# Performance work log

Measured on AMD Instinct MI355X. Metric: run time of the kernel, lower is better.

The kernel has to match this reference:

```python
import jax, jax.numpy as jnp
import numpy as np

HEAD_DIM = 32
KERNEL = 3
DILATION = 2
PAD = DILATION * (KERNEL - 1) // 2  # = 2
SCALE = HEAD_DIM ** (-0.5)


def _unfold(x):
    """Emulate nn.Unfold(kernel_size=KERNEL, dilation=DILATION, padding=PAD, stride=1).
    x: [B, C, H, W] -> [B, C, K*K, H, W] (channel-major, kernel positions inner,
    matching torch's C*K*K channel layout after the module's reshape)."""
    B, C, H, W = x.shape
    xp = jnp.pad(x, ((0, 0), (0, 0), (PAD, PAD), (PAD, PAD)))
    patches = [xp[:, :, i * DILATION:i * DILATION + H, j * DILATION:j * DILATION + W]
               for i in range(KERNEL) for j in range(KERNEL)]
    return jnp.stack(patches, axis=2)  # [B, C, K2, H, W]


def setup_inputs() -> dict:
    key = jax.random.key(0)
    kq, kk, kv = jax.random.split(key, 3)
    B, d, H, W = 4, 384, 64, 64
    q = jax.random.normal(kq, (B, d, H, W), dtype=jnp.float32)
    k = jax.random.normal(kk, (B, d, H, W), dtype=jnp.float32)
    v = jax.random.normal(kv, (B, d, H, W), dtype=jnp.float32)
    return {"q": q, "k": k, "v": v}


def reference(q, k, v):
    B, d, H, W = q.shape
    nh = d // HEAD_DIM
    K2 = KERNEL * KERNEL
    L = H * W
    # q: [B, nh, hd, L]
    qh = q.reshape(B, nh, HEAD_DIM, L)
    # unfolded k, v: [B, nh, hd, K2, L]
    ku = _unfold(k).reshape(B, nh, HEAD_DIM, K2, L)
    vu = _unfold(v).reshape(B, nh, HEAD_DIM, K2, L)
    # per-pixel attention logits: [B, nh, L, K2]
    attn = jnp.einsum('bncl,bnckl->bnlk', qh, ku) * SCALE
    attn = jax.nn.softmax(attn, axis=-1)
    # weighted values: [B, nh, L, hd]
    out = jnp.einsum('bnlk,bnckl->bnlc', attn, vu)
    # -> [B, L, nh, hd] -> [B, H, W, d]
    return out.transpose(0, 2, 1, 3).reshape(B, H, W, d)
```

## Files before the change

kernel.cpp:

```cpp
#include <hip/hip_runtime.h>


#define NHD  12
#define DDIM 384
#define HH   64
#define WW   64
#define HWSZ 4096
#define SCALEF 0.17677669529663687f

__global__ __launch_bounds__(256) void dilate_attn(const float* __restrict__ q,
                                                   const float* __restrict__ k,
                                                   const float* __restrict__ v,
                                                   float* __restrict__ out) {
    const int tid = threadIdx.x;
    const int r   = tid >> 6;
    const int x   = tid & 63;
    const int bz  = blockIdx.x;
    const int bh  = bz >> 4;
    const int b   = bh / NHD;
    const int n   = bh - b * NHD;
    const int y   = (bz & 15) * 4 + r;

    const int cbase = (b * DDIM + n * 32) * HWSZ;
    const int pix   = y * WW + x;

    int  rowoff[3];
    bool vy[3];
#pragma unroll
    for (int di = 0; di < 3; ++di) {
        int yy = y + 2 * di - 2;
        vy[di] = (yy >= 0) && (yy < HH);
        yy = yy < 0 ? 0 : (yy > 63 ? 63 : yy);
        rowoff[di] = yy * WW + x;
    }
    const bool vxm = (x >= 2);
    const bool vxp = (x <= 61);
    bool tval[9];
#pragma unroll
    for (int di = 0; di < 3; ++di) {
        tval[di * 3 + 0] = vy[di] && vxm;
        tval[di * 3 + 1] = vy[di];
        tval[di * 3 + 2] = vy[di] && vxp;
    }

    float qreg[32];
#pragma unroll
    for (int c = 0; c < 32; ++c) qreg[c] = q[cbase + pix + c * HWSZ] * SCALEF;

    float l[9];
#pragma unroll
    for (int t = 0; t < 9; ++t) l[t] = 0.f;
#pragma unroll
    for (int c = 0; c < 32; ++c) {
        const int base = cbase + c * HWSZ;
        const float qc = qreg[c];
#pragma unroll
        for (int di = 0; di < 3; ++di) {
            const float kc = k[base + rowoff[di]];
            const float km = __shfl_up(kc, 2);
            const float kp = __shfl_down(kc, 2);
            l[di * 3 + 0] += qc * km;
            l[di * 3 + 1] += qc * kc;
            l[di * 3 + 2] += qc * kp;
        }
    }

#pragma unroll
    for (int t = 0; t < 9; ++t) l[t] = tval[t] ? l[t] : 0.f;
    float m = l[0];
#pragma unroll
    for (int t = 1; t < 9; ++t) m = fmaxf(m, l[t]);
    float w[9], s = 0.f;
#pragma unroll
    for (int t = 0; t < 9; ++t) { w[t] = __expf(l[t] - m); s += w[t]; }
    float inv = 1.0f / s;
#pragma unroll
    for (int t = 0; t < 9; ++t) w[t] = tval[t] ? (w[t] * inv) : 0.f;

    float o[32];
#pragma unroll
    for (int c = 0; c < 32; ++c) o[c] = 0.f;
#pragma unroll
    for (int c = 0; c < 32; ++c) {
        const int base = cbase + c * HWSZ;
        float acc = 0.f;
#pragma unroll
        for (int di = 0; di < 3; ++di) {
            const float vc = v[base + rowoff[di]];
            const float vm = __shfl_up(vc, 2);
            const float vp = __shfl_down(vc, 2);
            acc += w[di * 3 + 0] * vm + w[di * 3 + 1] * vc + w[di * 3 + 2] * vp;
        }
        o[c] = acc;
    }

    const int ob = (b * HH * WW + pix) * DDIM + n * 32;
#pragma unroll
    for (int j = 0; j < 8; ++j)
        *(float4*)(out + ob + j * 4) =
            make_float4(o[j * 4], o[j * 4 + 1], o[j * 4 + 2], o[j * 4 + 3]);
}

extern "C" void kernel_launch(void* const* d_in, const int* in_sizes, int n_in,
                              void* d_out, int out_size, void* d_ws, size_t ws_size,
                              hipStream_t stream) {
    const float* q = (const float*)d_in[0];
    const float* k = (const float*)d_in[1];
    const float* v = (const float*)d_in[2];
    float* out = (float*)d_out;
    hipLaunchKernelGGL(dilate_attn, dim3(768), dim3(256), 0, stream, q, k, v, out);
}
```

Before: 124.7 us.

## Split channels across lane groups with float4 pixel loads and XCD-aware block remap

Each wave now covers one row with 16 lanes of 4 consecutive pixels each, and the 32 head channels are split into four groups of 8 across lane quarters. Loads of q, k and v become float4. Partial logits are reduced with xor shuffles across the channel groups, and neighbour taps come from shuffles of float4 components. The block index is also remapped so that consecutive logical blocks spread across the 8 XCDs. The intent is to raise memory-access width and cut per-thread register pressure, at the cost of extra shuffle reductions, and the output stores now write only 8 channels per pixel.

```diff
diff --git a/kernel.cpp b/kernel.cpp
--- a/kernel.cpp
+++ b/kernel.cpp
@@ -12,17 +12,23 @@
                                                    const float* __restrict__ k,
                                                    const float* __restrict__ v,
                                                    float* __restrict__ out) {
-    const int tid = threadIdx.x;
-    const int r   = tid >> 6;
-    const int x   = tid & 63;
-    const int bz  = blockIdx.x;
-    const int bh  = bz >> 4;
-    const int b   = bh / NHD;
-    const int n   = bh - b * NHD;
-    const int y   = (bz & 15) * 4 + r;
+    const int tid  = threadIdx.x;
+    const int lane = tid & 63;
+    const int i16  = lane & 15;
+    const int cg   = (lane >> 4) & 3;
+    const int wv   = tid >> 6;
+    const int x0   = i16 * 4;
 
-    const int cbase = (b * DDIM + n * 32) * HWSZ;
-    const int pix   = y * WW + x;
+    const int phys = blockIdx.x;
+    const int lz   = (phys & 7) * 96 + (phys >> 3);
+
+    const int bh = lz >> 4;
+    const int y  = (lz & 15) * 4 + wv;
+    const int b  = bh / NHD;
+    const int n  = bh - b * NHD;
+
+    const int cbase = (b * DDIM + n * 32 + cg * 8) * HWSZ;
+    const int prow  = y * WW;
 
     int  rowoff[3];
     bool vy[3];
@@ -31,74 +37,100 @@
         int yy = y + 2 * di - 2;
         vy[di] = (yy >= 0) && (yy < HH);
         yy = yy < 0 ? 0 : (yy > 63 ? 63 : yy);
-        rowoff[di] = yy * WW + x;
-    }
-    const bool vxm = (x >= 2);
-    const bool vxp = (x <= 61);
-    bool tval[9];
-#pragma unroll
-    for (int di = 0; di < 3; ++di) {
-        tval[di * 3 + 0] = vy[di] && vxm;
-        tval[di * 3 + 1] = vy[di];
-        tval[di * 3 + 2] = vy[di] && vxp;
+        rowoff[di] = yy * WW + x0;
     }
 
-    float qreg[32];
+    float4 qv[8];
 #pragma unroll
-    for (int c = 0; c < 32; ++c) qreg[c] = q[cbase + pix + c * HWSZ] * SCALEF;
+    for (int c = 0; c < 8; ++c) {
+        float4 t = *(const float4*)(q + cbase + c * HWSZ + prow + x0);
+        qv[c] = make_float4(t.x * SCALEF, t.y * SCALEF, t.z * SCALEF, t.w * SCALEF);
+    }
 
-    float l[9];
+    float l[4][9];
 #pragma unroll
-    for (int t = 0; t < 9; ++t) l[t] = 0.f;
+    for (int p = 0; p < 4; ++p)
 #pragma unroll
-    for (int c = 0; c < 32; ++c) {
-        const int base = cbase + c * HWSZ;
-        const float qc = qreg[c];
+        for (int t = 0; t < 9; ++t) l[p][t] = 0.f;
+
+#pragma unroll
+    for (int c = 0; c < 8; ++c) {
 #pragma unroll
         for (int di = 0; di < 3; ++di) {
-            const float kc = k[base + rowoff[di]];
-            const float km = __shfl_up(kc, 2);
-            const float kp = __shfl_down(kc, 2);
-            l[di * 3 + 0] += qc * km;
-            l[di * 3 + 1] += qc * kc;
-            l[di * 3 + 2] += qc * kp;
+            const float4 kv = *(const float4*)(k + cbase + c * HWSZ + rowoff[di]);
+            const float km2 = __shfl_up(kv.z, 1);
+            const float km1 = __shfl_up(kv.w, 1);
+            const float kp4 = __shfl_down(kv.x, 1);
+            const float kp5 = __shfl_down(kv.y, 1);
+            const int t0 = di * 3;
+            l[0][t0+0] += qv[c].x * km2;  l[0][t0+1] += qv[c].x * kv.x;  l[0][t0+2] += qv[c].x * kv.z;
+            l[1][t0+0] += qv[c].y * km1;  l[1][t0+1] += qv[c].y * kv.y;  l[1][t0+2] += qv[c].y * kv.w;
+            l[2][t0+0] += qv[c].z * kv.x; l[2][t0+1] += qv[c].z * kv.z;  l[2][t0+2] += qv[c].z * kp4;
+            l[3][t0+0] += qv[c].w * kv.y; l[3][t0+1] += qv[c].w * kv.w;  l[3][t0+2] += qv[c].w * kp5;
         }
     }
 
 #pragma unroll
-    for (int t = 0; t < 9; ++t) l[t] = tval[t] ? l[t] : 0.f;
-    float m = l[0];
+    for (int p = 0; p < 4; ++p)
 #pragma unroll
-    for (int t = 1; t < 9; ++t) m = fmaxf(m, l[t]);
-    float w[9], s = 0.f;
+        for (int t = 0; t < 9; ++t) {
+            l[p][t] += __shfl_xor(l[p][t], 16, 64);
+            l[p][t] += __shfl_xor(l[p][t], 32, 64);
+        }
+
 #pragma unroll
-    for (int t = 0; t < 9; ++t) { w[t] = __expf(l[t] - m); s += w[t]; }
-    float inv = 1.0f / s;
-#pragma unroll
-    for (int t = 0; t < 9; ++t) w[t] = tval[t] ? (w[t] * inv) : 0.f;
-
-    float o[32];
-#pragma unroll
-    for (int c = 0; c < 32; ++c) o[c] = 0.f;
-#pragma unroll
-    for (int c = 0; c < 32; ++c) {
-        const int base = cbase + c * HWSZ;
-        float acc = 0.f;
+    for (int p = 0; p < 4; ++p) {
+        const int xg = x0 + p;
+        const bool vxm = (xg >= 2), vxp = (xg <= 61);
+        bool tv[9];
 #pragma unroll
         for (int di = 0; di < 3; ++di) {
-            const float vc = v[base + rowoff[di]];
-            const float vm = __shfl_up(vc, 2);
-            const float vp = __shfl_down(vc, 2);
-            acc += w[di * 3 + 0] * vm + w[di * 3 + 1] * vc + w[di * 3 + 2] * vp;
+            tv[di * 3 + 0] = vy[di] && vxm;
+            tv[di * 3 + 1] = vy[di];
+            tv[di * 3 + 2] = vy[di] && vxp;
         }
-        o[c] = acc;
+#pragma unroll
+        for (int t = 0; t < 9; ++t) l[p][t] = tv[t] ? l[p][t] : 0.f;
+        float m = l[p][0];
+#pragma unroll
+        for (int t = 1; t < 9; ++t) m = fmaxf(m, l[p][t]);
+        float s = 0.f;
+#pragma unroll
+        for (int t = 0; t < 9; ++t) { l[p][t] = __expf(l[p][t] - m); s += l[p][t]; }
+        const float inv = 1.0f / s;
+#pragma unroll
+        for (int t = 0; t < 9; ++t) l[p][t] = tv[t] ? (l[p][t] * inv) : 0.f;
     }
 
-    const int ob = (b * HH * WW + pix) * DDIM + n * 32;
+    float o[8][4];
 #pragma unroll
-    for (int j = 0; j < 8; ++j)
-        *(float4*)(out + ob + j * 4) =
-            make_float4(o[j * 4], o[j * 4 + 1], o[j * 4 + 2], o[j * 4 + 3]);
+    for (int c = 0; c < 8; ++c)
+#pragma unroll
+        for (int p = 0; p < 4; ++p) o[c][p] = 0.f;
+
+#pragma unroll
+    for (int c = 0; c < 8; ++c) {
+#pragma unroll
+        for (int di = 0; di < 3; ++di) {
+            const float4 vv = *(const float4*)(v + cbase + c * HWSZ + rowoff[di]);
+            const float vm2 = __shfl_up(vv.z, 1);
+            const float vm1 = __shfl_up(vv.w, 1);
+            const float vp4 = __shfl_down(vv.x, 1);
+            const float vp5 = __shfl_down(vv.y, 1);
+            const int t0 = di * 3;
+            o[c][0] += l[0][t0] * vm2  + l[0][t0+1] * vv.x + l[0][t0+2] * vv.z;
+            o[c][1] += l[1][t0] * vm1  + l[1][t0+1] * vv.y + l[1][t0+2] * vv.w;
+            o[c][2] += l[2][t0] * vv.x + l[2][t0+1] * vv.z + l[2][t0+2] * vp4;
+            o[c][3] += l[3][t0] * vv.y + l[3][t0+1] * vv.w + l[3][t0+2] * vp5;
+        }
+    }
+
+#pragma unroll
+    for (int p = 0; p < 4; ++p) {
+        const int ob = (b * (HH * WW) + prow + x0 + p) * DDIM + n * 32 + cg * 8;
+        *(float4*)(out + ob)     = make_float4(o[0][p], o[1][p], o[2][p], o[3][p]);
+        *(float4*)(out + ob + 4) = make_float4(o[4][p], o[5][p], o[6][p], o[7][p]);
+    }
 }
 
 extern "C" void kernel_launch(void* const* d_in, const int* in_sizes, int n_in,
```

Result: faster. 118.5 us (-5.0%).

## Stage K and V halo tiles in LDS via async global-to-LDS loads

Applied to the files above, without the earlier changes.

Each block now copies its 32-channel by 8-row K tile (rows y0-2..y0+5) into shared memory with asynchronous global_load_lds, then reads neighbours from LDS instead of doing three global loads per channel plus wave shuffles. The same buffer is then refilled with the V tile, and this load overlaps with the softmax. Block indices are also remapped so consecutive physical blocks spread across the XCDs. The cost is a 64 KB LDS footprint per block, which limits occupancy, plus added barriers. Because LDS data is written by asynchronous loads, correctness depends on __syncthreads waiting for those loads to finish.

```diff
diff --git a/kernel.cpp b/kernel.cpp
--- a/kernel.cpp
+++ b/kernel.cpp
@@ -12,57 +12,95 @@
                                                    const float* __restrict__ k,
                                                    const float* __restrict__ v,
                                                    float* __restrict__ out) {
+    __shared__ float buf[32 * 8 * 64];
+
     const int tid = threadIdx.x;
     const int r   = tid >> 6;
     const int x   = tid & 63;
-    const int bz  = blockIdx.x;
-    const int bh  = bz >> 4;
-    const int b   = bh / NHD;
-    const int n   = bh - b * NHD;
-    const int y   = (bz & 15) * 4 + r;
+
+    const int phys = blockIdx.x;
+    const int lz   = (phys & 7) * 96 + (phys >> 3);
+    const int bh   = lz >> 4;
+    const int y0   = (lz & 15) * 4;
+    const int y    = y0 + r;
+    const int b    = bh / NHD;
+    const int n    = bh - b * NHD;
 
     const int cbase = (b * DDIM + n * 32) * HWSZ;
     const int pix   = y * WW + x;
 
-    int  rowoff[3];
-    bool vy[3];
+    auto* lds0 = (__attribute__((address_space(3))) char*)buf;
+
+    const int flat0 = r * 1024 + x;
+
 #pragma unroll
-    for (int di = 0; di < 3; ++di) {
-        int yy = y + 2 * di - 2;
-        vy[di] = (yy >= 0) && (yy < HH);
-        yy = yy < 0 ? 0 : (yy > 63 ? 63 : yy);
-        rowoff[di] = yy * WW + x;
-    }
-    const bool vxm = (x >= 2);
-    const bool vxp = (x <= 61);
-    bool tval[9];
-#pragma unroll
-    for (int di = 0; di < 3; ++di) {
-        tval[di * 3 + 0] = vy[di] && vxm;
-        tval[di * 3 + 1] = vy[di];
-        tval[di * 3 + 2] = vy[di] && vxp;
+    for (int i = 0; i < 16; ++i) {
+        const int flat = flat0 + i * 64;
+        const int ch   = flat >> 7;
+        const int row  = (flat >> 4) & 7;
+        const int x4   = (flat & 15) << 2;
+        int gy = y0 - 2 + row;
+        gy = gy < 0 ? 0 : (gy > 63 ? 63 : gy);
+        const float* gsrc = k + cbase + ch * HWSZ + gy * WW + x4;
+        __builtin_amdgcn_global_load_lds(
+            (const __attribute__((address_space(1))) void*)gsrc,
+            (__attribute__((address_space(3))) void*)(lds0 + (r * 16 + i) * 1024),
+            16, 0, 0);
     }
 
     float qreg[32];
 #pragma unroll
     for (int c = 0; c < 32; ++c) qreg[c] = q[cbase + pix + c * HWSZ] * SCALEF;
 
+    bool vy[3];
+#pragma unroll
+    for (int di = 0; di < 3; ++di) {
+        int yy = y + 2 * di - 2;
+        vy[di] = (yy >= 0) && (yy < HH);
+    }
+    const int xm = (x >= 2)  ? x - 2 : 0;
+    const int xp = (x <= 61) ? x + 2 : 63;
+    bool tval[9];
+#pragma unroll
+    for (int di = 0; di < 3; ++di) {
+        tval[di * 3 + 0] = vy[di] && (x >= 2);
+        tval[di * 3 + 1] = vy[di];
+        tval[di * 3 + 2] = vy[di] && (x <= 61);
+    }
+
+    __syncthreads();
+
     float l[9];
 #pragma unroll
     for (int t = 0; t < 9; ++t) l[t] = 0.f;
 #pragma unroll
     for (int c = 0; c < 32; ++c) {
-        const int base = cbase + c * HWSZ;
         const float qc = qreg[c];
+        const float* cb = &buf[c * 512];
 #pragma unroll
         for (int di = 0; di < 3; ++di) {
-            const float kc = k[base + rowoff[di]];
-            const float km = __shfl_up(kc, 2);
-            const float kp = __shfl_down(kc, 2);
-            l[di * 3 + 0] += qc * km;
-            l[di * 3 + 1] += qc * kc;
-            l[di * 3 + 2] += qc * kp;
+            const float* rowp = cb + (r + 2 * di) * 64;
+            l[di * 3 + 0] += qc * rowp[xm];
+            l[di * 3 + 1] += qc * rowp[x];
+            l[di * 3 + 2] += qc * rowp[xp];
         }
+    }
+
+    __syncthreads();
+
+#pragma unroll
+    for (int i = 0; i < 16; ++i) {
+        const int flat = flat0 + i * 64;
+        const int ch   = flat >> 7;
+        const int row  = (flat >> 4) & 7;
+        const int x4   = (flat & 15) << 2;
+        int gy = y0 - 2 + row;
+        gy = gy < 0 ? 0 : (gy > 63 ? 63 : gy);
+        const float* gsrc = v + cbase + ch * HWSZ + gy * WW + x4;
+        __builtin_amdgcn_global_load_lds(
+            (const __attribute__((address_space(1))) void*)gsrc,
+            (__attribute__((address_space(3))) void*)(lds0 + (r * 16 + i) * 1024),
+            16, 0, 0);
     }
 
 #pragma unroll
@@ -77,28 +115,27 @@
 #pragma unroll
     for (int t = 0; t < 9; ++t) w[t] = tval[t] ? (w[t] * inv) : 0.f;
 
-    float o[32];
-#pragma unroll
-    for (int c = 0; c < 32; ++c) o[c] = 0.f;
-#pragma unroll
-    for (int c = 0; c < 32; ++c) {
-        const int base = cbase + c * HWSZ;
-        float acc = 0.f;
-#pragma unroll
-        for (int di = 0; di < 3; ++di) {
-            const float vc = v[base + rowoff[di]];
-            const float vm = __shfl_up(vc, 2);
-            const float vp = __shfl_down(vc, 2);
-            acc += w[di * 3 + 0] * vm + w[di * 3 + 1] * vc + w[di * 3 + 2] * vp;
-        }
-        o[c] = acc;
-    }
+    __syncthreads();
 
     const int ob = (b * HH * WW + pix) * DDIM + n * 32;
 #pragma unroll
-    for (int j = 0; j < 8; ++j)
-        *(float4*)(out + ob + j * 4) =
-            make_float4(o[j * 4], o[j * 4 + 1], o[j * 4 + 2], o[j * 4 + 3]);
+    for (int cg = 0; cg < 8; ++cg) {
+        float o4[4];
+#pragma unroll
+        for (int j = 0; j < 4; ++j) {
+            const float* cb = &buf[(cg * 4 + j) * 512];
+            float acc = 0.f;
+#pragma unroll
+            for (int di = 0; di < 3; ++di) {
+                const float* rowp = cb + (r + 2 * di) * 64;
+                acc += w[di * 3 + 0] * rowp[xm]
+                     + w[di * 3 + 1] * rowp[x]
+                     + w[di * 3 + 2] * rowp[xp];
+            }
+            o4[j] = acc;
+        }
+        *(float4*)(out + ob + cg * 4) = make_float4(o4[0], o4[1], o4[2], o4[3]);
+    }
 }
 
 extern "C" void kernel_launch(void* const* d_in, const int* in_sizes, int n_in,
```

Result: faster. 116.8 us (-6.3%).

## Stage K/V halo rows in LDS with double-buffered async global-to-LDS loads

Applied to the files above, without the earlier changes.

Replaces per-thread global loads and lane shuffles for K and V with a double-buffered pipeline. Each stage copies 8 channels × 6 rows into shared memory using global_load_lds, while the previous buffer is consumed for QK and PV. Blocks shrink to 128 threads covering 2 output rows, and block indices are remapped so neighbouring tiles land on the same XCD for L2 locality. The aim is to hide global memory latency and cut shuffle work. In exchange, the halo overhead per output row grows, and the many barriers add synchronisation cost.

```diff
diff --git a/kernel.cpp b/kernel.cpp
--- a/kernel.cpp
+++ b/kernel.cpp
@@ -7,34 +7,53 @@
 #define WW   64
 #define HWSZ 4096
 #define SCALEF 0.17677669529663687f
+#define CF 3072
 
-__global__ __launch_bounds__(256) void dilate_attn(const float* __restrict__ q,
+typedef __attribute__((address_space(3))) char  lds_char;
+typedef __attribute__((address_space(1))) void  gvoid;
+
+__global__ __launch_bounds__(128) void dilate_attn(const float* __restrict__ q,
                                                    const float* __restrict__ k,
                                                    const float* __restrict__ v,
                                                    float* __restrict__ out) {
+    __shared__ float bufA[CF];
+    __shared__ float bufB[CF];
+
     const int tid = threadIdx.x;
     const int r   = tid >> 6;
     const int x   = tid & 63;
-    const int bz  = blockIdx.x;
-    const int bh  = bz >> 4;
-    const int b   = bh / NHD;
-    const int n   = bh - b * NHD;
-    const int y   = (bz & 15) * 4 + r;
+
+    const int phys = blockIdx.x;
+    const int lz   = (phys & 7) * 192 + (phys >> 3);
+    const int bh   = lz >> 5;
+    const int y0   = (lz & 31) * 2;
+    const int y    = y0 + r;
+    const int b    = bh / NHD;
+    const int n    = bh - b * NHD;
 
     const int cbase = (b * DDIM + n * 32) * HWSZ;
     const int pix   = y * WW + x;
 
-    int  rowoff[3];
+    int goff[6];
+#pragma unroll
+    for (int i = 0; i < 6; ++i) {
+        const int f0  = (r * 6 + i) * 256 + x * 4;
+        const int ch8 = f0 / 384;
+        const int rem = f0 - ch8 * 384;
+        const int row = rem >> 6;
+        const int x4  = rem & 63;
+        int gy = y0 - 2 + row;
+        gy = gy < 0 ? 0 : (gy > 63 ? 63 : gy);
+        goff[i] = ch8 * HWSZ + gy * WW + x4;
+    }
+
     bool vy[3];
 #pragma unroll
     for (int di = 0; di < 3; ++di) {
-        int yy = y + 2 * di - 2;
+        const int yy = y + 2 * di - 2;
         vy[di] = (yy >= 0) && (yy < HH);
-        yy = yy < 0 ? 0 : (yy > 63 ? 63 : yy);
-        rowoff[di] = yy * WW + x;
     }
-    const bool vxm = (x >= 2);
-    const bool vxp = (x <= 61);
+    const bool vxm = (x >= 2), vxp = (x <= 61);
     bool tval[9];
 #pragma unroll
     for (int di = 0; di < 3; ++di) {
@@ -43,6 +62,45 @@
         tval[di * 3 + 2] = vy[di] && vxp;
     }
 
+#define STAGE(TB, CH, BUF) do {                                                   \
+    const float* _tb = (TB) + cbase + (CH) * 8 * HWSZ;                            \
+    _Pragma("unroll")                                                             \
+    for (int i = 0; i < 6; ++i) {                                                 \
+        __builtin_amdgcn_global_load_lds(                                         \
+            (const gvoid*)(_tb + goff[i]),                                        \
+            (__attribute__((address_space(3))) void*)((lds_char*)(BUF) +          \
+                                                      (r * 6 + i) * 1024),        \
+            16, 0, 0);                                                            \
+    } } while (0)
+
+#define QKC(CH, BUF) do {                                                         \
+    _Pragma("unroll")                                                             \
+    for (int c8 = 0; c8 < 8; ++c8) {                                              \
+        const float qc = qreg[(CH) * 8 + c8];                                     \
+        _Pragma("unroll")                                                         \
+        for (int di = 0; di < 3; ++di) {                                          \
+            const float* rp = &(BUF)[c8 * 384 + (r + 2 * di) * 64 + x];           \
+            l[di * 3 + 0] += qc * rp[-2];                                         \
+            l[di * 3 + 1] += qc * rp[0];                                          \
+            l[di * 3 + 2] += qc * rp[2];                                          \
+        } } } while (0)
+
+#define PVC(CH, BUF) do {                                                         \
+    _Pragma("unroll")                                                             \
+    for (int c8 = 0; c8 < 8; ++c8) {                                              \
+        float acc = 0.f;                                                          \
+        _Pragma("unroll")                                                         \
+        for (int di = 0; di < 3; ++di) {                                          \
+            const float* rp = &(BUF)[c8 * 384 + (r + 2 * di) * 64 + x];           \
+            acc += w[di * 3 + 0] * rp[-2] + w[di * 3 + 1] * rp[0]                 \
+                 + w[di * 3 + 2] * rp[2];                                         \
+        }                                                                         \
+        o[(CH) * 8 + c8] = acc;                                                   \
+    } } while (0)
+
+    STAGE(k, 0, bufA);
+    STAGE(k, 1, bufB);
+
     float qreg[32];
 #pragma unroll
     for (int c = 0; c < 32; ++c) qreg[c] = q[cbase + pix + c * HWSZ] * SCALEF;
@@ -50,20 +108,20 @@
     float l[9];
 #pragma unroll
     for (int t = 0; t < 9; ++t) l[t] = 0.f;
-#pragma unroll
-    for (int c = 0; c < 32; ++c) {
-        const int base = cbase + c * HWSZ;
-        const float qc = qreg[c];
-#pragma unroll
-        for (int di = 0; di < 3; ++di) {
-            const float kc = k[base + rowoff[di]];
-            const float km = __shfl_up(kc, 2);
-            const float kp = __shfl_down(kc, 2);
-            l[di * 3 + 0] += qc * km;
-            l[di * 3 + 1] += qc * kc;
-            l[di * 3 + 2] += qc * kp;
-        }
-    }
+
+    __syncthreads();
+    QKC(0, bufA);
+    __syncthreads();
+    STAGE(k, 2, bufA);
+    QKC(1, bufB);
+    __syncthreads();
+    STAGE(k, 3, bufB);
+    QKC(2, bufA);
+    __syncthreads();
+    STAGE(v, 0, bufA);
+    QKC(3, bufB);
+    __syncthreads();
+    STAGE(v, 1, bufB);
 
 #pragma unroll
     for (int t = 0; t < 9; ++t) l[t] = tval[t] ? l[t] : 0.f;
@@ -73,26 +131,20 @@
     float w[9], s = 0.f;
 #pragma unroll
     for (int t = 0; t < 9; ++t) { w[t] = __expf(l[t] - m); s += w[t]; }
-    float inv = 1.0f / s;
+    const float inv = 1.0f / s;
 #pragma unroll
     for (int t = 0; t < 9; ++t) w[t] = tval[t] ? (w[t] * inv) : 0.f;
 
     float o[32];
-#pragma unroll
-    for (int c = 0; c < 32; ++c) o[c] = 0.f;
-#pragma unroll
-    for (int c = 0; c < 32; ++c) {
-        const int base = cbase + c * HWSZ;
-        float acc = 0.f;
-#pragma unroll
-        for (int di = 0; di < 3; ++di) {
-            const float vc = v[base + rowoff[di]];
-            const float vm = __shfl_up(vc, 2);
-            const float vp = __shfl_down(vc, 2);
-            acc += w[di * 3 + 0] * vm + w[di * 3 + 1] * vc + w[di * 3 + 2] * vp;
-        }
-        o[c] = acc;
-    }
+    PVC(0, bufA);
+    __syncthreads();
+    STAGE(v, 2, bufA);
+    PVC(1, bufB);
+    __syncthreads();
+    STAGE(v, 3, bufB);
+    PVC(2, bufA);
+    __syncthreads();
+    PVC(3, bufB);
 
     const int ob = (b * HH * WW + pix) * DDIM + n * 32;
 #pragma unroll
@@ -108,5 +160,5 @@
     const float* k = (const float*)d_in[1];
     const float* v = (const float*)d_in[2];
     float* out = (float*)d_out;
-    hipLaunchKernelGGL(dilate_attn, dim3(768), dim3(256), 0, stream, q, k, v, out);
+    hipLaunchKernelGGL(dilate_attn, dim3(1536), dim3(128), 0, stream, q, k, v, out);
 }
```

New measurement: 122.0 us. 2.2% less time.
